# Kernel optimization log

Measured on AMD Instinct MI355X. Metric: run time of the kernel, lower is better.

The kernel has to match this reference:

```python
import jax, jax.numpy as jnp
import numpy as np

N_NODES = 100000
N_EDGES = 1600000
NEG_SLOPE = 0.01  # nn.LeakyReLU default


def gcn_conv(x, edge_index, W, b, n_nodes):
    # PyG GCNConv: h = D^-1/2 (A+I) D^-1/2 (x W) + b
    h = x @ W  # [N, out]
    loops = jnp.arange(n_nodes, dtype=edge_index.dtype)
    src = jnp.concatenate([edge_index[0], loops])
    dst = jnp.concatenate([edge_index[1], loops])
    ones = jnp.ones(src.shape[0], dtype=h.dtype)
    deg = jax.ops.segment_sum(ones, dst, num_segments=n_nodes)  # in-degree incl. self-loop
    dinv = jnp.where(deg > 0, jax.lax.rsqrt(deg), 0.0)
    norm = dinv[src] * dinv[dst]  # [E+N]
    msg = h[src] * norm[:, None]  # gather + scale
    out = jax.ops.segment_sum(msg, dst, num_segments=n_nodes)  # scatter-add
    return out + b


def setup_inputs() -> dict:
    key = jax.random.key(0)
    ks = jax.random.split(key, 8)
    x = jax.random.normal(ks[0], (N_NODES, 128), dtype=jnp.float32)
    edge_index = jax.random.randint(ks[1], (2, N_EDGES), 0, N_NODES, dtype=jnp.int64)
    # Glorot-ish init for params
    W1 = jax.random.normal(ks[2], (128, 64), dtype=jnp.float32) / np.sqrt(128)
    b1 = jnp.zeros((64,), dtype=jnp.float32)
    W2 = jax.random.normal(ks[3], (64, 64), dtype=jnp.float32) / np.sqrt(64)
    b2 = jnp.zeros((64,), dtype=jnp.float32)
    Wfc = jax.random.normal(ks[4], (64, 4), dtype=jnp.float32) / np.sqrt(64)
    bfc = jnp.zeros((4,), dtype=jnp.float32)
    return {"x": x, "edge_index": edge_index, "W1": W1, "b1": b1,
            "W2": W2, "b2": b2, "Wfc": Wfc, "bfc": bfc}


def reference(x, edge_index, W1, b1, W2, b2, Wfc, bfc):
    h = gcn_conv(x, edge_index, W1, b1, N_NODES)
    h = jnp.where(h >= 0, h, NEG_SLOPE * h)  # LeakyReLU
    # F.dropout in eval mode -> identity
    h = gcn_conv(h, edge_index, W2, b2, N_NODES)
    out = h @ Wfc + bfc  # [N, 4]
    return out
```

## Files before the change

### kernel.cpp

```cpp
#include <hip/hip_runtime.h>

#define N_NODES 100000
#define N_EDGES 1600000
#define NEG_SLOPE 0.01f
#define NPAD 102400
#define NBLK_SCAN 391
#define NPART 16
#define PART_SZ 6250
#define CAPP 110000
#define BATCH1 1024
#define NBLK1 1563
#define DCHUNK 8
#define WIN_N 256
#define NWIN 25
#define CAP_B 4608
#define NBKT2 (NPART * NWIN)
#define BATCH1B 1024
#define CHUNK1B 108
#define NBLK1B (NPART * CHUNK1B)
#define CAP_WIN 4608
#define RCAP 768

__device__ inline unsigned pk_bf2(float lo, float hi) {
    unsigned a = __builtin_bit_cast(unsigned, lo);
    unsigned b = __builtin_bit_cast(unsigned, hi);
    a = (a + 0x7fffu + ((a >> 16) & 1u)) >> 16;
    b = (b + 0x7fffu + ((b >> 16) & 1u)) >> 16;
    return a | (b << 16);
}
__device__ inline float ub_lo(unsigned u) { return __builtin_bit_cast(float, u << 16); }
__device__ inline float ub_hi(unsigned u) { return __builtin_bit_cast(float, u & 0xffff0000u); }

__global__ void k_init(int* __restrict__ deg, int* __restrict__ gcur,
                       int* __restrict__ gcur2) {
    int i = blockIdx.x * 256 + threadIdx.x;
    if (i < NPAD) deg[i] = 0;
    if (i < NPART) gcur[i] = i * CAPP;
    if (i < NBKT2) gcur2[i] = i * CAP_B;
}

__global__ __launch_bounds__(256) void k_pass1(const int* __restrict__ src,
                                               const int* __restrict__ dst,
                                               int* __restrict__ gcur,
                                               unsigned* __restrict__ part) {
    __shared__ int hist[NPART];
    __shared__ int scanb[NPART];
    __shared__ int gbase[NPART];
    __shared__ int run[NPART];
    __shared__ unsigned stage[BATCH1];
    const int tid = threadIdx.x;
    const int lane = tid & 63;
    const int e0 = blockIdx.x * BATCH1;
    if (tid < NPART) hist[tid] = 0;
    __syncthreads();
    unsigned rec[4]; int bk[4], rk[4];
    unsigned long long mm[4];
#pragma unroll
    for (int i = 0; i < 4; ++i) {
        int e = e0 + i * 256 + tid;
        if (e < N_EDGES) {
            int d = dst[e];
            int s = src[e];
            int b = d / PART_SZ;
            bk[i] = b;
            rec[i] = ((unsigned)(d - b * PART_SZ) << 17) | (unsigned)s;
        } else bk[i] = -1;
        unsigned long long m = ~0ULL;
#pragma unroll
        for (int bit = 0; bit < 4; ++bit) {
            unsigned long long vote = __ballot((bk[i] >> bit) & 1);
            m &= ((bk[i] >> bit) & 1) ? vote : ~vote;
        }
        m &= __ballot(bk[i] >= 0);
        mm[i] = m;
        rk[i] = __popcll(m & ((1ULL << lane) - 1ULL));
        if (bk[i] >= 0 && rk[i] == 0)
            atomicAdd(&hist[bk[i]], __popcll(m));
    }
    __syncthreads();
    if (tid == 0) {
        int acc = 0;
        for (int b = 0; b < NPART; ++b) { scanb[b] = acc; acc += hist[b]; }
    }
    __syncthreads();
    if (tid < NPART) {
        gbase[tid] = atomicAdd(&gcur[tid], hist[tid]);
        run[tid] = 0;
    }
    __syncthreads();
#pragma unroll
    for (int i = 0; i < 4; ++i) {
        int base_ = 0;
        if (bk[i] >= 0 && rk[i] == 0)
            base_ = atomicAdd(&run[bk[i]], __popcll(mm[i]));
        int leader = mm[i] ? (__ffsll((unsigned long long)mm[i]) - 1) : 0;
        base_ = __shfl(base_, leader);
        if (bk[i] >= 0)
            stage[scanb[bk[i]] + base_ + rk[i]] = rec[i];
    }
    __syncthreads();
    for (int b = 0; b < NPART; ++b) {
        int len = hist[b], sb = scanb[b], gb = gbase[b];
        int lim = (b + 1) * CAPP - gb;
        if (len > lim) len = lim;
        for (int i = tid; i < len; i += 256)
            part[gb + i] = stage[sb + i];
    }
}

__global__ __launch_bounds__(256) void k_pass1b(const unsigned* __restrict__ part,
                                                const int* __restrict__ gcur,
                                                int* __restrict__ gcur2,
                                                unsigned* __restrict__ part2) {
    __shared__ int hist[NWIN];
    __shared__ int scanb[NWIN];
    __shared__ int gbase[NWIN];
    __shared__ int run[NWIN];
    __shared__ unsigned stage[BATCH1B];
    const int p = blockIdx.x & (NPART - 1);
    const int c = blockIdx.x >> 4;
    const int tid = threadIdx.x;
    const int base = p * CAPP;
    int pend = gcur[p]; if (pend > base + CAPP) pend = base + CAPP;
    const int rs = base + c * BATCH1B;
    int re = rs + BATCH1B; if (re > pend) re = pend;
    if (tid < NWIN) { hist[tid] = 0; run[tid] = 0; }
    __syncthreads();
    unsigned rec[4]; int wv[4];
#pragma unroll
    for (int i = 0; i < 4; ++i) {
        int idx = rs + i * 256 + tid;
        if (idx < re) {
            rec[i] = part[idx];
            wv[i] = (int)(rec[i] >> 17) >> 8;
            atomicAdd(&hist[wv[i]], 1);
        } else wv[i] = -1;
    }
    __syncthreads();
    if (tid == 0) {
        int acc = 0;
        for (int w = 0; w < NWIN; ++w) { scanb[w] = acc; acc += hist[w]; }
    }
    __syncthreads();
    if (tid < NWIN) gbase[tid] = atomicAdd(&gcur2[p * NWIN + tid], hist[tid]);
    __syncthreads();
#pragma unroll
    for (int i = 0; i < 4; ++i) {
        if (wv[i] >= 0) {
            int r = atomicAdd(&run[wv[i]], 1);
            stage[scanb[wv[i]] + r] = rec[i];
        }
    }
    __syncthreads();
    for (int w = 0; w < NWIN; ++w) {
        int len = hist[w], sb = scanb[w], gb = gbase[w];
        int lim = (p * NWIN + w + 1) * CAP_B - gb;
        if (len > lim) len = lim;
        for (int i = tid; i < len; i += 256)
            part2[gb + i] = stage[sb + i];
    }
}

__global__ __launch_bounds__(256) void k_degh(const unsigned* __restrict__ part,
                                              const int* __restrict__ gcur,
                                              int* __restrict__ deg) {
    __shared__ int hist[PART_SZ];
    const int p = blockIdx.x & (NPART - 1);
    const int q = blockIdx.x >> 4;
    const int base = p * CAPP;
    int end = gcur[p]; if (end > base + CAPP) end = base + CAPP;
    const int cnt = end - base;
    const int chunksz = (cnt + DCHUNK - 1) / DCHUNK;
    int rs = base + q * chunksz;
    int re = rs + chunksz; if (re > end) re = end;
    for (int i = threadIdx.x; i < PART_SZ; i += 256) hist[i] = 0;
    __syncthreads();
    for (int i = rs + threadIdx.x; i < re; i += 256)
        atomicAdd(&hist[part[i] >> 17], 1);
    __syncthreads();
    const int pbase = p * PART_SZ;
    for (int i = threadIdx.x; i < PART_SZ; i += 256) {
        int v = hist[i];
        if (v) atomicAdd(&deg[pbase + i], v);
    }
}

__global__ __launch_bounds__(256) void k_scan1(const int* __restrict__ deg,
                                               int* __restrict__ cur,
                                               int* __restrict__ bsum,
                                               float* __restrict__ dinv) {
    __shared__ int sd[256];
    int t = threadIdx.x;
    int gid = blockIdx.x * 256 + t;
    int v = (gid < N_NODES) ? deg[gid] : 0;
    dinv[gid] = rsqrtf((float)(v + 1));
    sd[t] = v;
    __syncthreads();
    for (int off = 1; off < 256; off <<= 1) {
        int add = (t >= off) ? sd[t - off] : 0;
        __syncthreads();
        sd[t] += add;
        __syncthreads();
    }
    cur[gid] = sd[t] - v;
    if (t == 255) bsum[blockIdx.x] = sd[255];
}
// ... 42 lines not shown
    if (tid == 0) {
        int acc = 0;
        for (int i = 0; i < nwin; ++i) { lofs[i] = acc; acc += lcnt[i]; }
        lofs[nwin] = acc;
    }
    __syncthreads();
    const int pbase = p * PART_SZ;
    const int wbase = cur[pbase + dlo];
    for (int i = bs + tid; i < be; i += 256) {
        unsigned rc = part2[i];
        int dl = (int)(rc >> 17);
        int s = rc & 0x1FFFF;
        int n = pbase + dl;
        float wgt = dinv[s] * dinv[n];
        int pos = lofs[dl - dlo] + atomicAdd(&lrun[dl - dlo], 1);
        uint2 r = make_uint2((unsigned)s, __builtin_bit_cast(unsigned, wgt));
        if (pos < CAP_WIN) stage[pos] = r;
        else csr8[wbase + pos] = r;
    }
    __syncthreads();
    int total = lofs[nwin]; if (total > CAP_WIN) total = CAP_WIN;
    for (int i = tid; i < total; i += 256)
        csr8[wbase + i] = stage[i];
}

__global__ __launch_bounds__(256) void k_gemm_bf(const float* __restrict__ X,
                                                 const float* __restrict__ W,
                                                 unsigned* __restrict__ Y) {
    __shared__ float ws[128 * 64];
    const int tid = threadIdx.x;
    const int row0 = blockIdx.x * 64;
    for (int i = tid; i < 2048; i += 256)
        ((float4*)ws)[i] = ((const float4*)W)[i];
    __syncthreads();
    const int cg = tid & 15, rg = tid >> 4;
    const int c0 = cg * 4;
    const float4* Xv = (const float4*)X;
    size_t rb0, rb1, rb2, rb3;
    {
        int row = row0 + rg * 4;
        rb0 = (size_t)((row     < N_NODES) ? row     : (N_NODES - 1)) * 32;
        rb1 = (size_t)((row + 1 < N_NODES) ? row + 1 : (N_NODES - 1)) * 32;
        rb2 = (size_t)((row + 2 < N_NODES) ? row + 2 : (N_NODES - 1)) * 32;
        rb3 = (size_t)((row + 3 < N_NODES) ? row + 3 : (N_NODES - 1)) * 32;
    }
    float acc[4][4] = {};
    float4 xa0 = Xv[rb0], xa1 = Xv[rb1], xa2 = Xv[rb2], xa3 = Xv[rb3];
#pragma unroll 1
    for (int kq = 0; kq < 32; kq += 2) {
        float4 xb0 = Xv[rb0 + kq + 1], xb1 = Xv[rb1 + kq + 1];
        float4 xb2 = Xv[rb2 + kq + 1], xb3 = Xv[rb3 + kq + 1];
        {
            const int k = kq * 4;
            float4 w0 = *(const float4*)&ws[(k + 0) * 64 + c0];
            float4 w1 = *(const float4*)&ws[(k + 1) * 64 + c0];
            float4 w2 = *(const float4*)&ws[(k + 2) * 64 + c0];
            float4 w3 = *(const float4*)&ws[(k + 3) * 64 + c0];
            float4 xv;
            xv = xa0;
            acc[0][0] = fmaf(xv.x, w0.x, acc[0][0]); acc[0][1] = fmaf(xv.x, w0.y, acc[0][1]);
            acc[0][2] = fmaf(xv.x, w0.z, acc[0][2]); acc[0][3] = fmaf(xv.x, w0.w, acc[0][3]);
            acc[0][0] = fmaf(xv.y, w1.x, acc[0][0]); acc[0][1] = fmaf(xv.y, w1.y, acc[0][1]);
            acc[0][2] = fmaf(xv.y, w1.z, acc[0][2]); acc[0][3] = fmaf(xv.y, w1.w, acc[0][3]);
            acc[0][0] = fmaf(xv.z, w2.x, acc[0][0]); acc[0][1] = fmaf(xv.z, w2.y, acc[0][1]);
            acc[0][2] = fmaf(xv.z, w2.z, acc[0][2]); acc[0][3] = fmaf(xv.z, w2.w, acc[0][3]);
            acc[0][0] = fmaf(xv.w, w3.x, acc[0][0]); acc[0][1] = fmaf(xv.w, w3.y, acc[0][1]);
            acc[0][2] = fmaf(xv.w, w3.z, acc[0][2]); acc[0][3] = fmaf(xv.w, w3.w, acc[0][3]);
            xv = xa1;
            acc[1][0] = fmaf(xv.x, w0.x, acc[1][0]); acc[1][1] = fmaf(xv.x, w0.y, acc[1][1]);
            acc[1][2] = fmaf(xv.x, w0.z, acc[1][2]); acc[1][3] = fmaf(xv.x, w0.w, acc[1][3]);
            acc[1][0] = fmaf(xv.y, w1.x, acc[1][0]); acc[1][1] = fmaf(xv.y, w1.y, acc[1][1]);
            acc[1][2] = fmaf(xv.y, w1.z, acc[1][2]); acc[1][3] = fmaf(xv.y, w1.w, acc[1][3]);
            acc[1][0] = fmaf(xv.z, w2.x, acc[1][0]); acc[1][1] = fmaf(xv.z, w2.y, acc[1][1]);
            acc[1][2] = fmaf(xv.z, w2.z, acc[1][2]); acc[1][3] = fmaf(xv.z, w2.w, acc[1][3]);
            acc[1][0] = fmaf(xv.w, w3.x, acc[1][0]); acc[1][1] = fmaf(xv.w, w3.y, acc[1][1]);
            acc[1][2] = fmaf(xv.w, w3.z, acc[1][2]); acc[1][3] = fmaf(xv.w, w3.w, acc[1][3]);
            xv = xa2;
            acc[2][0] = fmaf(xv.x, w0.x, acc[2][0]); acc[2][1] = fmaf(xv.x, w0.y, acc[2][1]);
            acc[2][2] = fmaf(xv.x, w0.z, acc[2][2]); acc[2][3] = fmaf(xv.x, w0.w, acc[2][3]);
            acc[2][0] = fmaf(xv.y, w1.x, acc[2][0]); acc[2][1] = fmaf(xv.y, w1.y, acc[2][1]);
            acc[2][2] = fmaf(xv.y, w1.z, acc[2][2]); acc[2][3] = fmaf(xv.y, w1.w, acc[2][3]);
            acc[2][0] = fmaf(xv.z, w2.x, acc[2][0]); acc[2][1] = fmaf(xv.z, w2.y, acc[2][1]);
            acc[2][2] = fmaf(xv.z, w2.z, acc[2][2]); acc[2][3] = fmaf(xv.z, w2.w, acc[2][3]);
            acc[2][0] = fmaf(xv.w, w3.x, acc[2][0]); acc[2][1] = fmaf(xv.w, w3.y, acc[2][1]);
            acc[2][2] = fmaf(xv.w, w3.z, acc[2][2]); acc[2][3] = fmaf(xv.w, w3.w, acc[2][3]);
            xv = xa3;
            acc[3][0] = fmaf(xv.x, w0.x, acc[3][0]); acc[3][1] = fmaf(xv.x, w0.y, acc[3][1]);
            acc[3][2] = fmaf(xv.x, w0.z, acc[3][2]); acc[3][3] = fmaf(xv.x, w0.w, acc[3][3]);
            acc[3][0] = fmaf(xv.y, w1.x, acc[3][0]); acc[3][1] = fmaf(xv.y, w1.y, acc[3][1]);
            acc[3][2] = fmaf(xv.y, w1.z, acc[3][2]); acc[3][3] = fmaf(xv.y, w1.w, acc[3][3]);
            acc[3][0] = fmaf(xv.z, w2.x, acc[3][0]); acc[3][1] = fmaf(xv.z, w2.y, acc[3][1]);
            acc[3][2] = fmaf(xv.z, w2.z, acc[3][2]); acc[3][3] = fmaf(xv.z, w2.w, acc[3][3]);
            acc[3][0] = fmaf(xv.w, w3.x, acc[3][0]); acc[3][1] = fmaf(xv.w, w3.y, acc[3][1]);
            acc[3][2] = fmaf(xv.w, w3.z, acc[3][2]); acc[3][3] = fmaf(xv.w, w3.w, acc[3][3]);
        }
        if (kq + 2 < 32) {
            xa0 = Xv[rb0 + kq + 2]; xa1 = Xv[rb1 + kq + 2];
            xa2 = Xv[rb2 + kq + 2]; xa3 = Xv[rb3 + kq + 2];
        }
        {
            const int k = (kq + 1) * 4;
            float4 w0 = *(const float4*)&ws[(k + 0) * 64 + c0];
            float4 w1 = *(const float4*)&ws[(k + 1) * 64 + c0];
            float4 w2 = *(const float4*)&ws[(k + 2) * 64 + c0];
            float4 w3 = *(const float4*)&ws[(k + 3) * 64 + c0];
            float4 xv;
            xv = xb0;
            acc[0][0] = fmaf(xv.x, w0.x, acc[0][0]); acc[0][1] = fmaf(xv.x, w0.y, acc[0][1]);
            acc[0][2] = fmaf(xv.x, w0.z, acc[0][2]); acc[0][3] = fmaf(xv.x, w0.w, acc[0][3]);
            acc[0][0] = fmaf(xv.y, w1.x, acc[0][0]); acc[0][1] = fmaf(xv.y, w1.y, acc[0][1]);
            acc[0][2] = fmaf(xv.y, w1.z, acc[0][2]); acc[0][3] = fmaf(xv.y, w1.w, acc[0][3]);
            acc[0][0] = fmaf(xv.z, w2.x, acc[0][0]); acc[0][1] = fmaf(xv.z, w2.y, acc[0][1]);
            acc[0][2] = fmaf(xv.z, w2.z, acc[0][2]); acc[0][3] = fmaf(xv.z, w2.w, acc[0][3]);
            acc[0][0] = fmaf(xv.w, w3.x, acc[0][0]); acc[0][1] = fmaf(xv.w, w3.y, acc[0][1]);
            acc[0][2] = fmaf(xv.w, w3.z, acc[0][2]); acc[0][3] = fmaf(xv.w, w3.w, acc[0][3]);
            xv = xb1;
            acc[1][0] = fmaf(xv.x, w0.x, acc[1][0]); acc[1][1] = fmaf(xv.x, w0.y, acc[1][1]);
            acc[1][2] = fmaf(xv.x, w0.z, acc[1][2]); acc[1][3] = fmaf(xv.x, w0.w, acc[1][3]);
            acc[1][0] = fmaf(xv.y, w1.x, acc[1][0]); acc[1][1] = fmaf(xv.y, w1.y, acc[1][1]);
            acc[1][2] = fmaf(xv.y, w1.z, acc[1][2]); acc[1][3] = fmaf(xv.y, w1.w, acc[1][3]);
            acc[1][0] = fmaf(xv.z, w2.x, acc[1][0]); acc[1][1] = fmaf(xv.z, w2.y, acc[1][1]);
            acc[1][2] = fmaf(xv.z, w2.z, acc[1][2]); acc[1][3] = fmaf(xv.z, w2.w, acc[1][3]);
            acc[1][0] = fmaf(xv.w, w3.x, acc[1][0]); acc[1][1] = fmaf(xv.w, w3.y, acc[1][1]);
            acc[1][2] = fmaf(xv.w, w3.z, acc[1][2]); acc[1][3] = fmaf(xv.w, w3.w, acc[1][3]);
            xv = xb2;
            acc[2][0] = fmaf(xv.x, w0.x, acc[2][0]); acc[2][1] = fmaf(xv.x, w0.y, acc[2][1]);
            acc[2][2] = fmaf(xv.x, w0.z, acc[2][2]); acc[2][3] = fmaf(xv.x, w0.w, acc[2][3]);
            acc[2][0] = fmaf(xv.y, w1.x, acc[2][0]); acc[2][1] = fmaf(xv.y, w1.y, acc[2][1]);
            acc[2][2] = fmaf(xv.y, w1.z, acc[2][2]); acc[2][3] = fmaf(xv.y, w1.w, acc[2][3]);
            acc[2][0] = fmaf(xv.z, w2.x, acc[2][0]); acc[2][1] = fmaf(xv.z, w2.y, acc[2][1]);
            acc[2][2] = fmaf(xv.z, w2.z, acc[2][2]); acc[2][3] = fmaf(xv.z, w2.w, acc[2][3]);
            acc[2][0] = fmaf(xv.w, w3.x, acc[2][0]); acc[2][1] = fmaf(xv.w, w3.y, acc[2][1]);
            acc[2][2] = fmaf(xv.w, w3.z, acc[2][2]); acc[2][3] = fmaf(xv.w, w3.w, acc[2][3]);
            xv = xb3;
            acc[3][0] = fmaf(xv.x, w0.x, acc[3][0]); acc[3][1] = fmaf(xv.x, w0.y, acc[3][1]);
            acc[3][2] = fmaf(xv.x, w0.z, acc[3][2]); acc[3][3] = fmaf(xv.x, w0.w, acc[3][3]);
            acc[3][0] = fmaf(xv.y, w1.x, acc[3][0]); acc[3][1] = fmaf(xv.y, w1.y, acc[3][1]);
            acc[3][2] = fmaf(xv.y, w1.z, acc[3][2]); acc[3][3] = fmaf(xv.y, w1.w, acc[3][3]);
            acc[3][0] = fmaf(xv.z, w2.x, acc[3][0]); acc[3][1] = fmaf(xv.z, w2.y, acc[3][1]);
            acc[3][2] = fmaf(xv.z, w2.z, acc[3][2]); acc[3][3] = fmaf(xv.z, w2.w, acc[3][3]);
            acc[3][0] = fmaf(xv.w, w3.x, acc[3][0]); acc[3][1] = fmaf(xv.w, w3.y, acc[3][1]);
            acc[3][2] = fmaf(xv.w, w3.z, acc[3][2]); acc[3][3] = fmaf(xv.w, w3.w, acc[3][3]);
        }
    }
#pragma unroll
    for (int j = 0; j < 4; ++j) {
        int row = row0 + rg * 4 + j;
        if (row < N_NODES) {
            uint2 v;
            v.x = pk_bf2(acc[j][0], acc[j][1]);
            v.y = pk_bf2(acc[j][2], acc[j][3]);
            *(uint2*)&Y[(size_t)row * 32 + cg * 2] = v;
        }
    }
}

__global__ __launch_bounds__(256) void k_foldw(const float* __restrict__ W2,
                                               const float* __restrict__ b2,
                                               const float* __restrict__ Wfc,
                                               const float* __restrict__ bfc,
                                               float* __restrict__ Wc,
                                               float* __restrict__ cfold) {
    __shared__ float wf[64 * 4];
    int tid = threadIdx.x;
    wf[tid] = Wfc[tid];
    __syncthreads();
    int k = tid >> 2, c = tid & 3;
    float acc = 0.f;
#pragma unroll
    for (int j = 0; j < 64; ++j) acc = fmaf(W2[k * 64 + j], wf[j * 4 + c], acc);
    Wc[k * 4 + c] = acc;
    if (tid < 4) {
        float s = bfc[tid];
        for (int j = 0; j < 64; ++j) s = fmaf(b2[j], wf[j * 4 + tid], s);
        cfold[tid] = s;
    }
}

__global__ __launch_bounds__(256) void k_agg_bf2(const int* __restrict__ cur,
                                                 const uint2* __restrict__ csr8,
                                                 const float* __restrict__ dinv,
                                                 const unsigned* __restrict__ hb,
                                                 const float* __restrict__ b,
                                                 const float* __restrict__ Wc,
                                                 float* __restrict__ G) {
    __shared__ uint2 rec[RCAP];
    __shared__ int scur[17];
    const int tid = threadIdx.x;
    const int base = blockIdx.x * 16;
    if (tid < 17) scur[tid] = cur[base + tid];
    __syncthreads();
    const int bstart = scur[0];
    const int total = scur[16] - bstart;
    const int staged = (total < RCAP) ? total : RCAP;
    for (int i = tid; i < staged; i += 256) rec[i] = csr8[bstart + i];
    __syncthreads();
    const int lane = tid & 63, wv = tid >> 6;
    const int sub = lane & 31, half = lane >> 5;
    for (int nn = wv; nn < 16; nn += 4) {
// ... 190 lines not shown
    const float* W2  = (const float*)d_in[4];
    const float* b2  = (const float*)d_in[5];
    const float* Wfc = (const float*)d_in[6];
    const float* bfc = (const float*)d_in[7];
    float* out = (float*)d_out;

    int*      deg   = (int*)d_ws;
    int*      cur   = deg + NPAD;
    float*    dinv  = (float*)(cur + NPAD);
    int*      bsum  = (int*)(dinv + NPAD);
    float*    Wc    = (float*)(bsum + 1024);
    float*    cfold = Wc + 256;
    int*      gcur  = (int*)(cfold + 256);
    int*      gcur2 = gcur + 256;
    unsigned* part  = (unsigned*)(gcur2 + 512);
    unsigned* part2 = part + (size_t)NPART * CAPP;
    uint2*    csr8  = (uint2*)(part2 + (size_t)NBKT2 * CAP_B);
    unsigned* hb    = (unsigned*)(csr8 + N_EDGES);
    float*    G     = (float*)(hb + (size_t)N_NODES * 32);

    const int* src = ei;
    const int* dst = ei + N_EDGES;

    k_init<<<(NPAD + 255) / 256, 256, 0, stream>>>(deg, gcur, gcur2);

    k_pass1<<<NBLK1, 256, 0, stream>>>(src, dst, gcur, part);

    k_pass1b<<<NBLK1B, 256, 0, stream>>>(part, gcur, gcur2, part2);

    k_degh<<<NPART * DCHUNK, 256, 0, stream>>>(part, gcur, deg);

    k_scan1<<<NBLK_SCAN, 256, 0, stream>>>(deg, cur, bsum, dinv);
    k_scan2<<<1, 512, 0, stream>>>(bsum);
    k_scan3<<<NBLK_SCAN, 256, 0, stream>>>(cur, bsum);

    k_pass2c<<<NBKT2, 256, 0, stream>>>(part2, gcur2, dinv, cur, csr8);

    k_foldw<<<1, 256, 0, stream>>>(W2, b2, Wfc, bfc, Wc, cfold);

    k_gemm_bf<<<(N_NODES + 63) / 64, 256, 0, stream>>>(x, W1, hb);
    k_agg_bf2<<<N_NODES / 16, 256, 0, stream>>>(cur, csr8, dinv, hb, b1, Wc, G);

    k_agg4<<<(N_NODES + 255) / 256, 256, 0, stream>>>(cur, csr8, dinv,
                                                      (const float4*)G, cfold,
                                                      (float4*)out);
}
```

Baseline: 175.7 us.

## Merge independent kernels into shared launches via block-index dispatch

Independent stages are combined into single launches whose blocks branch on blockIdx. The weight-folding kernel joins the init kernel, the GEMM on x joins the first partition pass, and the second partition pass joins the degree histogram. This cuts the number of launches and lets unrelated work overlap on the device. The cost is higher shared-memory and register demand in the combined kernels, since each block must reserve the larger footprint, which may lower occupancy for the lighter branch.

```diff
diff --git a/kernel.cpp b/kernel.cpp
--- a/kernel.cpp
+++ b/kernel.cpp
@@ -10,14 +10,14 @@
 #define CAPP 110000
 #define BATCH1 1024
 #define NBLK1 1563
+#define NBLKG 1563
 #define DCHUNK 8
 #define WIN_N 256
 #define NWIN 25
 #define CAP_B 4608
 #define NBKT2 (NPART * NWIN)
 #define BATCH1B 1024
-#define CHUNK1B 108
-#define NBLK1B (NPART * CHUNK1B)
+#define NBLK1B 1728
 #define CAP_WIN 4608
 #define RCAP 768
 
@@ -31,157 +31,314 @@
 __device__ inline float ub_lo(unsigned u) { return __builtin_bit_cast(float, u << 16); }
 __device__ inline float ub_hi(unsigned u) { return __builtin_bit_cast(float, u & 0xffff0000u); }
 
-__global__ void k_init(int* __restrict__ deg, int* __restrict__ gcur,
-                       int* __restrict__ gcur2) {
-    int i = blockIdx.x * 256 + threadIdx.x;
-    if (i < NPAD) deg[i] = 0;
-    if (i < NPART) gcur[i] = i * CAPP;
-    if (i < NBKT2) gcur2[i] = i * CAP_B;
-}
-
-__global__ __launch_bounds__(256) void k_pass1(const int* __restrict__ src,
-                                               const int* __restrict__ dst,
-                                               int* __restrict__ gcur,
-                                               unsigned* __restrict__ part) {
-    __shared__ int hist[NPART];
-    __shared__ int scanb[NPART];
-    __shared__ int gbase[NPART];
-    __shared__ int run[NPART];
-    __shared__ unsigned stage[BATCH1];
+__global__ __launch_bounds__(256) void k_init(int* __restrict__ deg,
+                                              int* __restrict__ gcur,
+                                              int* __restrict__ gcur2,
+                                              const float* __restrict__ W2,
+                                              const float* __restrict__ b2,
+                                              const float* __restrict__ Wfc,
+                                              const float* __restrict__ bfc,
+                                              float* __restrict__ Wc,
+                                              float* __restrict__ cfold) {
+    __shared__ float wf[64 * 4];
     const int tid = threadIdx.x;
-    const int lane = tid & 63;
-    const int e0 = blockIdx.x * BATCH1;
-    if (tid < NPART) hist[tid] = 0;
-    __syncthreads();
-    unsigned rec[4]; int bk[4], rk[4];
-    unsigned long long mm[4];
-#pragma unroll
-    for (int i = 0; i < 4; ++i) {
-        int e = e0 + i * 256 + tid;
-        if (e < N_EDGES) {
-            int d = dst[e];
-            int s = src[e];
-            int b = d / PART_SZ;
-            bk[i] = b;
-            rec[i] = ((unsigned)(d - b * PART_SZ) << 17) | (unsigned)s;
-        } else bk[i] = -1;
-        unsigned long long m = ~0ULL;
-#pragma unroll
-        for (int bit = 0; bit < 4; ++bit) {
-            unsigned long long vote = __ballot((bk[i] >> bit) & 1);
-            m &= ((bk[i] >> bit) & 1) ? vote : ~vote;
-        }
-        m &= __ballot(bk[i] >= 0);
-        mm[i] = m;
-        rk[i] = __popcll(m & ((1ULL << lane) - 1ULL));
-        if (bk[i] >= 0 && rk[i] == 0)
-            atomicAdd(&hist[bk[i]], __popcll(m));
-    }
-    __syncthreads();
-    if (tid == 0) {
-        int acc = 0;
-        for (int b = 0; b < NPART; ++b) { scanb[b] = acc; acc += hist[b]; }
-    }
-    __syncthreads();
-    if (tid < NPART) {
-        gbase[tid] = atomicAdd(&gcur[tid], hist[tid]);
-        run[tid] = 0;
-    }
-    __syncthreads();
-#pragma unroll
-    for (int i = 0; i < 4; ++i) {
-        int base_ = 0;
-        if (bk[i] >= 0 && rk[i] == 0)
-            base_ = atomicAdd(&run[bk[i]], __popcll(mm[i]));
-        int leader = mm[i] ? (__ffsll((unsigned long long)mm[i]) - 1) : 0;
-        base_ = __shfl(base_, leader);
-        if (bk[i] >= 0)
-            stage[scanb[bk[i]] + base_ + rk[i]] = rec[i];
-    }
-    __syncthreads();
-    for (int b = 0; b < NPART; ++b) {
-        int len = hist[b], sb = scanb[b], gb = gbase[b];
-        int lim = (b + 1) * CAPP - gb;
-        if (len > lim) len = lim;
-        for (int i = tid; i < len; i += 256)
-            part[gb + i] = stage[sb + i];
-    }
-}
-
-__global__ __launch_bounds__(256) void k_pass1b(const unsigned* __restrict__ part,
-                                                const int* __restrict__ gcur,
-                                                int* __restrict__ gcur2,
-                                                unsigned* __restrict__ part2) {
-    __shared__ int hist[NWIN];
-    __shared__ int scanb[NWIN];
-    __shared__ int gbase[NWIN];
-    __shared__ int run[NWIN];
-    __shared__ unsigned stage[BATCH1B];
-    const int p = blockIdx.x & (NPART - 1);
-    const int c = blockIdx.x >> 4;
+    if (blockIdx.x < 400) {
+        int i = blockIdx.x * 256 + tid;
+        if (i < NPAD) deg[i] = 0;
+        if (i < NPART) gcur[i] = i * CAPP;
+        if (i < NBKT2) gcur2[i] = i * CAP_B;
+    } else {
+        wf[tid] = Wfc[tid];
+        __syncthreads();
+        int k = tid >> 2, c = tid & 3;
+        float acc = 0.f;
+#pragma unroll
+        for (int j = 0; j < 64; ++j) acc = fmaf(W2[k * 64 + j], wf[j * 4 + c], acc);
+        Wc[k * 4 + c] = acc;
+        if (tid < 4) {
+            float s = bfc[tid];
+            for (int j = 0; j < 64; ++j) s = fmaf(b2[j], wf[j * 4 + tid], s);
+            cfold[tid] = s;
+        }
+    }
+}
+
+__global__ __launch_bounds__(256) void k_p1gemm(const int* __restrict__ src,
+                                                const int* __restrict__ dst,
+                                                int* __restrict__ gcur,
+                                                unsigned* __restrict__ part,
+                                                const float* __restrict__ X,
+                                                const float* __restrict__ W,
+                                                unsigned* __restrict__ Y) {
+    __shared__ __align__(16) unsigned smem[8192];
     const int tid = threadIdx.x;
-    const int base = p * CAPP;
-    int pend = gcur[p]; if (pend > base + CAPP) pend = base + CAPP;
-    const int rs = base + c * BATCH1B;
-    int re = rs + BATCH1B; if (re > pend) re = pend;
-    if (tid < NWIN) { hist[tid] = 0; run[tid] = 0; }
-    __syncthreads();
-    unsigned rec[4]; int wv[4];
-#pragma unroll
-    for (int i = 0; i < 4; ++i) {
-        int idx = rs + i * 256 + tid;
-        if (idx < re) {
-            rec[i] = part[idx];
-            wv[i] = (int)(rec[i] >> 17) >> 8;
-            atomicAdd(&hist[wv[i]], 1);
-        } else wv[i] = -1;
-    }
-    __syncthreads();
-    if (tid == 0) {
-        int acc = 0;
-        for (int w = 0; w < NWIN; ++w) { scanb[w] = acc; acc += hist[w]; }
-    }
-    __syncthreads();
-    if (tid < NWIN) gbase[tid] = atomicAdd(&gcur2[p * NWIN + tid], hist[tid]);
-    __syncthreads();
-#pragma unroll
-    for (int i = 0; i < 4; ++i) {
-        if (wv[i] >= 0) {
-            int r = atomicAdd(&run[wv[i]], 1);
-            stage[scanb[wv[i]] + r] = rec[i];
-        }
-    }
-    __syncthreads();
-    for (int w = 0; w < NWIN; ++w) {
-        int len = hist[w], sb = scanb[w], gb = gbase[w];
-        int lim = (p * NWIN + w + 1) * CAP_B - gb;
-        if (len > lim) len = lim;
-        for (int i = tid; i < len; i += 256)
-            part2[gb + i] = stage[sb + i];
-    }
-}
-
-__global__ __launch_bounds__(256) void k_degh(const unsigned* __restrict__ part,
-                                              const int* __restrict__ gcur,
-                                              int* __restrict__ deg) {
-    __shared__ int hist[PART_SZ];
-    const int p = blockIdx.x & (NPART - 1);
-    const int q = blockIdx.x >> 4;
-    const int base = p * CAPP;
-    int end = gcur[p]; if (end > base + CAPP) end = base + CAPP;
-    const int cnt = end - base;
-    const int chunksz = (cnt + DCHUNK - 1) / DCHUNK;
-    int rs = base + q * chunksz;
-    int re = rs + chunksz; if (re > end) re = end;
-    for (int i = threadIdx.x; i < PART_SZ; i += 256) hist[i] = 0;
-    __syncthreads();
-    for (int i = rs + threadIdx.x; i < re; i += 256)
-        atomicAdd(&hist[part[i] >> 17], 1);
-    __syncthreads();
-    const int pbase = p * PART_SZ;
-    for (int i = threadIdx.x; i < PART_SZ; i += 256) {
-        int v = hist[i];
-        if (v) atomicAdd(&deg[pbase + i], v);
+    if (blockIdx.x < NBLK1) {
+        int* hist  = (int*)smem;
+        int* scanb = hist + 16;
+        int* gbase = hist + 32;
+        int* run   = hist + 48;
+        unsigned* stage = smem + 64;
+        const int lane = tid & 63;
+        const int e0 = blockIdx.x * BATCH1;
+        if (tid < NPART) hist[tid] = 0;
+        __syncthreads();
+        unsigned rec[4]; int bk[4], rk[4];
+        unsigned long long mm[4];
+#pragma unroll
+        for (int i = 0; i < 4; ++i) {
+            int e = e0 + i * 256 + tid;
+            if (e < N_EDGES) {
+                int d = dst[e];
+                int s = src[e];
+                int b = d / PART_SZ;
+                bk[i] = b;
+                rec[i] = ((unsigned)(d - b * PART_SZ) << 17) | (unsigned)s;
+            } else bk[i] = -1;
+            unsigned long long m = ~0ULL;
+#pragma unroll
+            for (int bit = 0; bit < 4; ++bit) {
+                unsigned long long vote = __ballot((bk[i] >> bit) & 1);
+                m &= ((bk[i] >> bit) & 1) ? vote : ~vote;
+            }
+            m &= __ballot(bk[i] >= 0);
+            mm[i] = m;
+            rk[i] = __popcll(m & ((1ULL << lane) - 1ULL));
+            if (bk[i] >= 0 && rk[i] == 0)
+                atomicAdd(&hist[bk[i]], __popcll(m));
+        }
+        __syncthreads();
+        if (tid == 0) {
+            int acc = 0;
+            for (int b = 0; b < NPART; ++b) { scanb[b] = acc; acc += hist[b]; }
+        }
+        __syncthreads();
+        if (tid < NPART) {
+            gbase[tid] = atomicAdd(&gcur[tid], hist[tid]);
+            run[tid] = 0;
+        }
+        __syncthreads();
+#pragma unroll
+        for (int i = 0; i < 4; ++i) {
+            int base_ = 0;
+            if (bk[i] >= 0 && rk[i] == 0)
+                base_ = atomicAdd(&run[bk[i]], __popcll(mm[i]));
+            int leader = mm[i] ? (__ffsll((unsigned long long)mm[i]) - 1) : 0;
+            base_ = __shfl(base_, leader);
+            if (bk[i] >= 0)
+                stage[scanb[bk[i]] + base_ + rk[i]] = rec[i];
+        }
+        __syncthreads();
+        for (int b = 0; b < NPART; ++b) {
+            int len = hist[b], sb = scanb[b], gb = gbase[b];
+            int lim = (b + 1) * CAPP - gb;
+            if (len > lim) len = lim;
+            for (int i = tid; i < len; i += 256)
+                part[gb + i] = stage[sb + i];
+        }
+    } else {
+        float* ws = (float*)smem;
+        const int row0 = (blockIdx.x - NBLK1) * 64;
+        for (int i = tid; i < 2048; i += 256)
+            ((float4*)ws)[i] = ((const float4*)W)[i];
+        __syncthreads();
+        const int cg = tid & 15, rg = tid >> 4;
+        const int c0 = cg * 4;
+        const float4* Xv = (const float4*)X;
+        size_t rb0, rb1, rb2, rb3;
+        {
+            int row = row0 + rg * 4;
+            rb0 = (size_t)((row     < N_NODES) ? row     : (N_NODES - 1)) * 32;
+            rb1 = (size_t)((row + 1 < N_NODES) ? row + 1 : (N_NODES - 1)) * 32;
+            rb2 = (size_t)((row + 2 < N_NODES) ? row + 2 : (N_NODES - 1)) * 32;
+            rb3 = (size_t)((row + 3 < N_NODES) ? row + 3 : (N_NODES - 1)) * 32;
+        }
+        float acc[4][4] = {};
+        float4 xa0 = Xv[rb0], xa1 = Xv[rb1], xa2 = Xv[rb2], xa3 = Xv[rb3];
+#pragma unroll 1
+        for (int kq = 0; kq < 32; kq += 2) {
+            float4 xb0 = Xv[rb0 + kq + 1], xb1 = Xv[rb1 + kq + 1];
+            float4 xb2 = Xv[rb2 + kq + 1], xb3 = Xv[rb3 + kq + 1];
+            {
+                const int k = kq * 4;
+                float4 w0 = *(const float4*)&ws[(k + 0) * 64 + c0];
+                float4 w1 = *(const float4*)&ws[(k + 1) * 64 + c0];
+                float4 w2 = *(const float4*)&ws[(k + 2) * 64 + c0];
+                float4 w3 = *(const float4*)&ws[(k + 3) * 64 + c0];
+                float4 xv;
+                xv = xa0;
+                acc[0][0] = fmaf(xv.x, w0.x, acc[0][0]); acc[0][1] = fmaf(xv.x, w0.y, acc[0][1]);
+                acc[0][2] = fmaf(xv.x, w0.z, acc[0][2]); acc[0][3] = fmaf(xv.x, w0.w, acc[0][3]);
+                acc[0][0] = fmaf(xv.y, w1.x, acc[0][0]); acc[0][1] = fmaf(xv.y, w1.y, acc[0][1]);
+                acc[0][2] = fmaf(xv.y, w1.z, acc[0][2]); acc[0][3] = fmaf(xv.y, w1.w, acc[0][3]);
+                acc[0][0] = fmaf(xv.z, w2.x, acc[0][0]); acc[0][1] = fmaf(xv.z, w2.y, acc[0][1]);
+                acc[0][2] = fmaf(xv.z, w2.z, acc[0][2]); acc[0][3] = fmaf(xv.z, w2.w, acc[0][3]);
+                acc[0][0] = fmaf(xv.w, w3.x, acc[0][0]); acc[0][1] = fmaf(xv.w, w3.y, acc[0][1]);
+                acc[0][2] = fmaf(xv.w, w3.z, acc[0][2]); acc[0][3] = fmaf(xv.w, w3.w, acc[0][3]);
+                xv = xa1;
+                acc[1][0] = fmaf(xv.x, w0.x, acc[1][0]); acc[1][1] = fmaf(xv.x, w0.y, acc[1][1]);
+                acc[1][2] = fmaf(xv.x, w0.z, acc[1][2]); acc[1][3] = fmaf(xv.x, w0.w, acc[1][3]);
+                acc[1][0] = fmaf(xv.y, w1.x, acc[1][0]); acc[1][1] = fmaf(xv.y, w1.y, acc[1][1]);
+                acc[1][2] = fmaf(xv.y, w1.z, acc[1][2]); acc[1][3] = fmaf(xv.y, w1.w, acc[1][3]);
+                acc[1][0] = fmaf(xv.z, w2.x, acc[1][0]); acc[1][1] = fmaf(xv.z, w2.y, acc[1][1]);
+                acc[1][2] = fmaf(xv.z, w2.z, acc[1][2]); acc[1][3] = fmaf(xv.z, w2.w, acc[1][3]);
+                acc[1][0] = fmaf(xv.w, w3.x, acc[1][0]); acc[1][1] = fmaf(xv.w, w3.y, acc[1][1]);
+                acc[1][2] = fmaf(xv.w, w3.z, acc[1][2]); acc[1][3] = fmaf(xv.w, w3.w, acc[1][3]);
+                xv = xa2;
+                acc[2][0] = fmaf(xv.x, w0.x, acc[2][0]); acc[2][1] = fmaf(xv.x, w0.y, acc[2][1]);
+                acc[2][2] = fmaf(xv.x, w0.z, acc[2][2]); acc[2][3] = fmaf(xv.x, w0.w, acc[2][3]);
+                acc[2][0] = fmaf(xv.y, w1.x, acc[2][0]); acc[2][1] = fmaf(xv.y, w1.y, acc[2][1]);
+                acc[2][2] = fmaf(xv.y, w1.z, acc[2][2]); acc[2][3] = fmaf(xv.y, w1.w, acc[2][3]);
+                acc[2][0] = fmaf(xv.z, w2.x, acc[2][0]); acc[2][1] = fmaf(xv.z, w2.y, acc[2][1]);
+                acc[2][2] = fmaf(xv.z, w2.z, acc[2][2]); acc[2][3] = fmaf(xv.z, w2.w, acc[2][3]);
+                acc[2][0] = fmaf(xv.w, w3.x, acc[2][0]); acc[2][1] = fmaf(xv.w, w3.y, acc[2][1]);
+                acc[2][2] = fmaf(xv.w, w3.z, acc[2][2]); acc[2][3] = fmaf(xv.w, w3.w, acc[2][3]);
+                xv = xa3;
+                acc[3][0] = fmaf(xv.x, w0.x, acc[3][0]); acc[3][1] = fmaf(xv.x, w0.y, acc[3][1]);
+                acc[3][2] = fmaf(xv.x, w0.z, acc[3][2]); acc[3][3] = fmaf(xv.x, w0.w, acc[3][3]);
+                acc[3][0] = fmaf(xv.y, w1.x, acc[3][0]); acc[3][1] = fmaf(xv.y, w1.y, acc[3][1]);
+                acc[3][2] = fmaf(xv.y, w1.z, acc[3][2]); acc[3][3] = fmaf(xv.y, w1.w, acc[3][3]);
+                acc[3][0] = fmaf(xv.z, w2.x, acc[3][0]); acc[3][1] = fmaf(xv.z, w2.y, acc[3][1]);
+                acc[3][2] = fmaf(xv.z, w2.z, acc[3][2]); acc[3][3] = fmaf(xv.z, w2.w, acc[3][3]);
+                acc[3][0] = fmaf(xv.w, w3.x, acc[3][0]); acc[3][1] = fmaf(xv.w, w3.y, acc[3][1]);
+                acc[3][2] = fmaf(xv.w, w3.z, acc[3][2]); acc[3][3] = fmaf(xv.w, w3.w, acc[3][3]);
+            }
+            if (kq + 2 < 32) {
+                xa0 = Xv[rb0 + kq + 2]; xa1 = Xv[rb1 + kq + 2];
+                xa2 = Xv[rb2 + kq + 2]; xa3 = Xv[rb3 + kq + 2];
+            }
+            {
+                const int k = (kq + 1) * 4;
+                float4 w0 = *(const float4*)&ws[(k + 0) * 64 + c0];
+                float4 w1 = *(const float4*)&ws[(k + 1) * 64 + c0];
+                float4 w2 = *(const float4*)&ws[(k + 2) * 64 + c0];
+                float4 w3 = *(const float4*)&ws[(k + 3) * 64 + c0];
+                float4 xv;
+                xv = xb0;
+                acc[0][0] = fmaf(xv.x, w0.x, acc[0][0]); acc[0][1] = fmaf(xv.x, w0.y, acc[0][1]);
+                acc[0][2] = fmaf(xv.x, w0.z, acc[0][2]); acc[0][3] = fmaf(xv.x, w0.w, acc[0][3]);
+                acc[0][0] = fmaf(xv.y, w1.x, acc[0][0]); acc[0][1] = fmaf(xv.y, w1.y, acc[0][1]);
+                acc[0][2] = fmaf(xv.y, w1.z, acc[0][2]); acc[0][3] = fmaf(xv.y, w1.w, acc[0][3]);
+                acc[0][0] = fmaf(xv.z, w2.x, acc[0][0]); acc[0][1] = fmaf(xv.z, w2.y, acc[0][1]);
+                acc[0][2] = fmaf(xv.z, w2.z, acc[0][2]); acc[0][3] = fmaf(xv.z, w2.w, acc[0][3]);
+                acc[0][0] = fmaf(xv.w, w3.x, acc[0][0]); acc[0][1] = fmaf(xv.w, w3.y, acc[0][1]);
+                acc[0][2] = fmaf(xv.w, w3.z, acc[0][2]); acc[0][3] = fmaf(xv.w, w3.w, acc[0][3]);
+                xv = xb1;
+                acc[1][0] = fmaf(xv.x, w0.x, acc[1][0]); acc[1][1] = fmaf(xv.x, w0.y, acc[1][1]);
+                acc[1][2] = fmaf(xv.x, w0.z, acc[1][2]); acc[1][3] = fmaf(xv.x, w0.w, acc[1][3]);
+                acc[1][0] = fmaf(xv.y, w1.x, acc[1][0]); acc[1][1] = fmaf(xv.y, w1.y, acc[1][1]);
+                acc[1][2] = fmaf(xv.y, w1.z, acc[1][2]); acc[1][3] = fmaf(xv.y, w1.w, acc[1][3]);
+                acc[1][0] = fmaf(xv.z, w2.x, acc[1][0]); acc[1][1] = fmaf(xv.z, w2.y, acc[1][1]);
+                acc[1][2] = fmaf(xv.z, w2.z, acc[1][2]); acc[1][3] = fmaf(xv.z, w2.w, acc[1][3]);
+                acc[1][0] = fmaf(xv.w, w3.x, acc[1][0]); acc[1][1] = fmaf(xv.w, w3.y, acc[1][1]);
+                acc[1][2] = fmaf(xv.w, w3.z, acc[1][2]); acc[1][3] = fmaf(xv.w, w3.w, acc[1][3]);
+                xv = xb2;
+                acc[2][0] = fmaf(xv.x, w0.x, acc[2][0]); acc[2][1] = fmaf(xv.x, w0.y, acc[2][1]);
+                acc[2][2] = fmaf(xv.x, w0.z, acc[2][2]); acc[2][3] = fmaf(xv.x, w0.w, acc[2][3]);
+                acc[2][0] = fmaf(xv.y, w1.x, acc[2][0]); acc[2][1] = fmaf(xv.y, w1.y, acc[2][1]);
+                acc[2][2] = fmaf(xv.y, w1.z, acc[2][2]); acc[2][3] = fmaf(xv.y, w1.w, acc[2][3]);
+                acc[2][0] = fmaf(xv.z, w2.x, acc[2][0]); acc[2][1] = fmaf(xv.z, w2.y, acc[2][1]);
+                acc[2][2] = fmaf(xv.z, w2.z, acc[2][2]); acc[2][3] = fmaf(xv.z, w2.w, acc[2][3]);
+                acc[2][0] = fmaf(xv.w, w3.x, acc[2][0]); acc[2][1] = fmaf(xv.w, w3.y, acc[2][1]);
+                acc[2][2] = fmaf(xv.w, w3.z, acc[2][2]); acc[2][3] = fmaf(xv.w, w3.w, acc[2][3]);
+                xv = xb3;
+                acc[3][0] = fmaf(xv.x, w0.x, acc[3][0]); acc[3][1] = fmaf(xv.x, w0.y, acc[3][1]);
+                acc[3][2] = fmaf(xv.x, w0.z, acc[3][2]); acc[3][3] = fmaf(xv.x, w0.w, acc[3][3]);
+                acc[3][0] = fmaf(xv.y, w1.x, acc[3][0]); acc[3][1] = fmaf(xv.y, w1.y, acc[3][1]);
+                acc[3][2] = fmaf(xv.y, w1.z, acc[3][2]); acc[3][3] = fmaf(xv.y, w1.w, acc[3][3]);
+                acc[3][0] = fmaf(xv.z, w2.x, acc[3][0]); acc[3][1] = fmaf(xv.z, w2.y, acc[3][1]);
+                acc[3][2] = fmaf(xv.z, w2.z, acc[3][2]); acc[3][3] = fmaf(xv.z, w2.w, acc[3][3]);
+                acc[3][0] = fmaf(xv.w, w3.x, acc[3][0]); acc[3][1] = fmaf(xv.w, w3.y, acc[3][1]);
+                acc[3][2] = fmaf(xv.w, w3.z, acc[3][2]); acc[3][3] = fmaf(xv.w, w3.w, acc[3][3]);
+            }
+        }
+#pragma unroll
+        for (int j = 0; j < 4; ++j) {
+            int row = row0 + rg * 4 + j;
+            if (row < N_NODES) {
+                uint2 v;
+                v.x = pk_bf2(acc[j][0], acc[j][1]);
+                v.y = pk_bf2(acc[j][2], acc[j][3]);
+                *(uint2*)&Y[(size_t)row * 32 + cg * 2] = v;
+            }
+        }
+    }
+}
+
+__global__ __launch_bounds__(256) void k_p1bdegh(const unsigned* __restrict__ part,
+                                                 const int* __restrict__ gcur,
+                                                 int* __restrict__ gcur2,
+                                                 unsigned* __restrict__ part2,
+                                                 int* __restrict__ deg) {
+    __shared__ __align__(16) int smem[PART_SZ];
+    const int tid = threadIdx.x;
+    if (blockIdx.x < NBLK1B) {
+        int* hist  = smem;
+        int* scanb = smem + 32;
+        int* gbase = smem + 64;
+        int* run   = smem + 96;
+        unsigned* stage = (unsigned*)(smem + 128);
+        const int p = blockIdx.x & (NPART - 1);
+        const int c = blockIdx.x >> 4;
+        const int base = p * CAPP;
+        int pend = gcur[p]; if (pend > base + CAPP) pend = base + CAPP;
+        const int rs = base + c * BATCH1B;
+        int re = rs + BATCH1B; if (re > pend) re = pend;
+        if (tid < NWIN) { hist[tid] = 0; run[tid] = 0; }
+        __syncthreads();
+        unsigned rec[4]; int wv[4];
+#pragma unroll
+        for (int i = 0; i < 4; ++i) {
+            int idx = rs + i * 256 + tid;
+            if (idx < re) {
+                rec[i] = part[idx];
+                wv[i] = (int)(rec[i] >> 17) >> 8;
+                atomicAdd(&hist[wv[i]], 1);
+            } else wv[i] = -1;
+        }
+        __syncthreads();
+        if (tid == 0) {
+            int acc = 0;
+            for (int w = 0; w < NWIN; ++w) { scanb[w] = acc; acc += hist[w]; }
+        }
+        __syncthreads();
+        if (tid < NWIN) gbase[tid] = atomicAdd(&gcur2[p * NWIN + tid], hist[tid]);
+        __syncthreads();
+#pragma unroll
+        for (int i = 0; i < 4; ++i) {
+            if (wv[i] >= 0) {
+                int r = atomicAdd(&run[wv[i]], 1);
+                stage[scanb[wv[i]] + r] = rec[i];
+            }
+        }
+        __syncthreads();
+        for (int w = 0; w < NWIN; ++w) {
+            int len = hist[w], sb = scanb[w], gb = gbase[w];
+            int lim = (p * NWIN + w + 1) * CAP_B - gb;
+            if (len > lim) len = lim;
+            for (int i = tid; i < len; i += 256)
+                part2[gb + i] = stage[sb + i];
+        }
+    } else {
+        int* hist = smem;
+        const int b2 = blockIdx.x - NBLK1B;
+        const int p = b2 & (NPART - 1);
+        const int q = b2 >> 4;
+        const int base = p * CAPP;
+        int end = gcur[p]; if (end > base + CAPP) end = base + CAPP;
+        const int cnt = end - base;
+        const int chunksz = (cnt + DCHUNK - 1) / DCHUNK;
+        int rs = base + q * chunksz;
+        int re = rs + chunksz; if (re > end) re = end;
+        for (int i = tid; i < PART_SZ; i += 256) hist[i] = 0;
+        __syncthreads();
+        for (int i = rs + tid; i < re; i += 256)
+            atomicAdd(&hist[part[i] >> 17], 1);
+        __syncthreads();
+        const int pbase = p * PART_SZ;
+        for (int i = tid; i < PART_SZ; i += 256) {
+            int v = hist[i];
+            if (v) atomicAdd(&deg[pbase + i], v);
+        }
     }
 }
 
@@ -270,159 +427,6 @@
     int total = lofs[nwin]; if (total > CAP_WIN) total = CAP_WIN;
     for (int i = tid; i < total; i += 256)
         csr8[wbase + i] = stage[i];
-}
-
-__global__ __launch_bounds__(256) void k_gemm_bf(const float* __restrict__ X,
-                                                 const float* __restrict__ W,
-                                                 unsigned* __restrict__ Y) {
-    __shared__ float ws[128 * 64];
-    const int tid = threadIdx.x;
-    const int row0 = blockIdx.x * 64;
-    for (int i = tid; i < 2048; i += 256)
-        ((float4*)ws)[i] = ((const float4*)W)[i];
-    __syncthreads();
-    const int cg = tid & 15, rg = tid >> 4;
-    const int c0 = cg * 4;
-    const float4* Xv = (const float4*)X;
-    size_t rb0, rb1, rb2, rb3;
-    {
-        int row = row0 + rg * 4;
-        rb0 = (size_t)((row     < N_NODES) ? row     : (N_NODES - 1)) * 32;
-        rb1 = (size_t)((row + 1 < N_NODES) ? row + 1 : (N_NODES - 1)) * 32;
-        rb2 = (size_t)((row + 2 < N_NODES) ? row + 2 : (N_NODES - 1)) * 32;
-        rb3 = (size_t)((row + 3 < N_NODES) ? row + 3 : (N_NODES - 1)) * 32;
-    }
-    float acc[4][4] = {};
-    float4 xa0 = Xv[rb0], xa1 = Xv[rb1], xa2 = Xv[rb2], xa3 = Xv[rb3];
-#pragma unroll 1
-    for (int kq = 0; kq < 32; kq += 2) {
-        float4 xb0 = Xv[rb0 + kq + 1], xb1 = Xv[rb1 + kq + 1];
-        float4 xb2 = Xv[rb2 + kq + 1], xb3 = Xv[rb3 + kq + 1];
-        {
-            const int k = kq * 4;
-            float4 w0 = *(const float4*)&ws[(k + 0) * 64 + c0];
-            float4 w1 = *(const float4*)&ws[(k + 1) * 64 + c0];
-            float4 w2 = *(const float4*)&ws[(k + 2) * 64 + c0];
-            float4 w3 = *(const float4*)&ws[(k + 3) * 64 + c0];
-            float4 xv;
-            xv = xa0;
-            acc[0][0] = fmaf(xv.x, w0.x, acc[0][0]); acc[0][1] = fmaf(xv.x, w0.y, acc[0][1]);
-            acc[0][2] = fmaf(xv.x, w0.z, acc[0][2]); acc[0][3] = fmaf(xv.x, w0.w, acc[0][3]);
-            acc[0][0] = fmaf(xv.y, w1.x, acc[0][0]); acc[0][1] = fmaf(xv.y, w1.y, acc[0][1]);
-            acc[0][2] = fmaf(xv.y, w1.z, acc[0][2]); acc[0][3] = fmaf(xv.y, w1.w, acc[0][3]);
-            acc[0][0] = fmaf(xv.z, w2.x, acc[0][0]); acc[0][1] = fmaf(xv.z, w2.y, acc[0][1]);
-            acc[0][2] = fmaf(xv.z, w2.z, acc[0][2]); acc[0][3] = fmaf(xv.z, w2.w, acc[0][3]);
-            acc[0][0] = fmaf(xv.w, w3.x, acc[0][0]); acc[0][1] = fmaf(xv.w, w3.y, acc[0][1]);
-            acc[0][2] = fmaf(xv.w, w3.z, acc[0][2]); acc[0][3] = fmaf(xv.w, w3.w, acc[0][3]);
-            xv = xa1;
-            acc[1][0] = fmaf(xv.x, w0.x, acc[1][0]); acc[1][1] = fmaf(xv.x, w0.y, acc[1][1]);
-            acc[1][2] = fmaf(xv.x, w0.z, acc[1][2]); acc[1][3] = fmaf(xv.x, w0.w, acc[1][3]);
-            acc[1][0] = fmaf(xv.y, w1.x, acc[1][0]); acc[1][1] = fmaf(xv.y, w1.y, acc[1][1]);
-            acc[1][2] = fmaf(xv.y, w1.z, acc[1][2]); acc[1][3] = fmaf(xv.y, w1.w, acc[1][3]);
-            acc[1][0] = fmaf(xv.z, w2.x, acc[1][0]); acc[1][1] = fmaf(xv.z, w2.y, acc[1][1]);
-            acc[1][2] = fmaf(xv.z, w2.z, acc[1][2]); acc[1][3] = fmaf(xv.z, w2.w, acc[1][3]);
-            acc[1][0] = fmaf(xv.w, w3.x, acc[1][0]); acc[1][1] = fmaf(xv.w, w3.y, acc[1][1]);
-            acc[1][2] = fmaf(xv.w, w3.z, acc[1][2]); acc[1][3] = fmaf(xv.w, w3.w, acc[1][3]);
-            xv = xa2;
-            acc[2][0] = fmaf(xv.x, w0.x, acc[2][0]); acc[2][1] = fmaf(xv.x, w0.y, acc[2][1]);
-            acc[2][2] = fmaf(xv.x, w0.z, acc[2][2]); acc[2][3] = fmaf(xv.x, w0.w, acc[2][3]);
-            acc[2][0] = fmaf(xv.y, w1.x, acc[2][0]); acc[2][1] = fmaf(xv.y, w1.y, acc[2][1]);
-            acc[2][2] = fmaf(xv.y, w1.z, acc[2][2]); acc[2][3] = fmaf(xv.y, w1.w, acc[2][3]);
-            acc[2][0] = fmaf(xv.z, w2.x, acc[2][0]); acc[2][1] = fmaf(xv.z, w2.y, acc[2][1]);
-            acc[2][2] = fmaf(xv.z, w2.z, acc[2][2]); acc[2][3] = fmaf(xv.z, w2.w, acc[2][3]);
-            acc[2][0] = fmaf(xv.w, w3.x, acc[2][0]); acc[2][1] = fmaf(xv.w, w3.y, acc[2][1]);
-            acc[2][2] = fmaf(xv.w, w3.z, acc[2][2]); acc[2][3] = fmaf(xv.w, w3.w, acc[2][3]);
-            xv = xa3;
-            acc[3][0] = fmaf(xv.x, w0.x, acc[3][0]); acc[3][1] = fmaf(xv.x, w0.y, acc[3][1]);
-            acc[3][2] = fmaf(xv.x, w0.z, acc[3][2]); acc[3][3] = fmaf(xv.x, w0.w, acc[3][3]);
-            acc[3][0] = fmaf(xv.y, w1.x, acc[3][0]); acc[3][1] = fmaf(xv.y, w1.y, acc[3][1]);
-            acc[3][2] = fmaf(xv.y, w1.z, acc[3][2]); acc[3][3] = fmaf(xv.y, w1.w, acc[3][3]);
-            acc[3][0] = fmaf(xv.z, w2.x, acc[3][0]); acc[3][1] = fmaf(xv.z, w2.y, acc[3][1]);
-            acc[3][2] = fmaf(xv.z, w2.z, acc[3][2]); acc[3][3] = fmaf(xv.z, w2.w, acc[3][3]);
-            acc[3][0] = fmaf(xv.w, w3.x, acc[3][0]); acc[3][1] = fmaf(xv.w, w3.y, acc[3][1]);
-            acc[3][2] = fmaf(xv.w, w3.z, acc[3][2]); acc[3][3] = fmaf(xv.w, w3.w, acc[3][3]);
-        }
-        if (kq + 2 < 32) {
-            xa0 = Xv[rb0 + kq + 2]; xa1 = Xv[rb1 + kq + 2];
-            xa2 = Xv[rb2 + kq + 2]; xa3 = Xv[rb3 + kq + 2];
-        }
-        {
-            const int k = (kq + 1) * 4;
-            float4 w0 = *(const float4*)&ws[(k + 0) * 64 + c0];
-            float4 w1 = *(const float4*)&ws[(k + 1) * 64 + c0];
-            float4 w2 = *(const float4*)&ws[(k + 2) * 64 + c0];
-            float4 w3 = *(const float4*)&ws[(k + 3) * 64 + c0];
-            float4 xv;
-            xv = xb0;
-            acc[0][0] = fmaf(xv.x, w0.x, acc[0][0]); acc[0][1] = fmaf(xv.x, w0.y, acc[0][1]);
-            acc[0][2] = fmaf(xv.x, w0.z, acc[0][2]); acc[0][3] = fmaf(xv.x, w0.w, acc[0][3]);
-            acc[0][0] = fmaf(xv.y, w1.x, acc[0][0]); acc[0][1] = fmaf(xv.y, w1.y, acc[0][1]);
-            acc[0][2] = fmaf(xv.y, w1.z, acc[0][2]); acc[0][3] = fmaf(xv.y, w1.w, acc[0][3]);
-            acc[0][0] = fmaf(xv.z, w2.x, acc[0][0]); acc[0][1] = fmaf(xv.z, w2.y, acc[0][1]);
-            acc[0][2] = fmaf(xv.z, w2.z, acc[0][2]); acc[0][3] = fmaf(xv.z, w2.w, acc[0][3]);
-            acc[0][0] = fmaf(xv.w, w3.x, acc[0][0]); acc[0][1] = fmaf(xv.w, w3.y, acc[0][1]);
-            acc[0][2] = fmaf(xv.w, w3.z, acc[0][2]); acc[0][3] = fmaf(xv.w, w3.w, acc[0][3]);
-            xv = xb1;
-            acc[1][0] = fmaf(xv.x, w0.x, acc[1][0]); acc[1][1] = fmaf(xv.x, w0.y, acc[1][1]);
-            acc[1][2] = fmaf(xv.x, w0.z, acc[1][2]); acc[1][3] = fmaf(xv.x, w0.w, acc[1][3]);
-            acc[1][0] = fmaf(xv.y, w1.x, acc[1][0]); acc[1][1] = fmaf(xv.y, w1.y, acc[1][1]);
-            acc[1][2] = fmaf(xv.y, w1.z, acc[1][2]); acc[1][3] = fmaf(xv.y, w1.w, acc[1][3]);
-            acc[1][0] = fmaf(xv.z, w2.x, acc[1][0]); acc[1][1] = fmaf(xv.z, w2.y, acc[1][1]);
-            acc[1][2] = fmaf(xv.z, w2.z, acc[1][2]); acc[1][3] = fmaf(xv.z, w2.w, acc[1][3]);
-            acc[1][0] = fmaf(xv.w, w3.x, acc[1][0]); acc[1][1] = fmaf(xv.w, w3.y, acc[1][1]);
-            acc[1][2] = fmaf(xv.w, w3.z, acc[1][2]); acc[1][3] = fmaf(xv.w, w3.w, acc[1][3]);
-            xv = xb2;
-            acc[2][0] = fmaf(xv.x, w0.x, acc[2][0]); acc[2][1] = fmaf(xv.x, w0.y, acc[2][1]);
-            acc[2][2] = fmaf(xv.x, w0.z, acc[2][2]); acc[2][3] = fmaf(xv.x, w0.w, acc[2][3]);
-            acc[2][0] = fmaf(xv.y, w1.x, acc[2][0]); acc[2][1] = fmaf(xv.y, w1.y, acc[2][1]);
-            acc[2][2] = fmaf(xv.y, w1.z, acc[2][2]); acc[2][3] = fmaf(xv.y, w1.w, acc[2][3]);
-            acc[2][0] = fmaf(xv.z, w2.x, acc[2][0]); acc[2][1] = fmaf(xv.z, w2.y, acc[2][1]);
-            acc[2][2] = fmaf(xv.z, w2.z, acc[2][2]); acc[2][3] = fmaf(xv.z, w2.w, acc[2][3]);
-            acc[2][0] = fmaf(xv.w, w3.x, acc[2][0]); acc[2][1] = fmaf(xv.w, w3.y, acc[2][1]);
-            acc[2][2] = fmaf(xv.w, w3.z, acc[2][2]); acc[2][3] = fmaf(xv.w, w3.w, acc[2][3]);
-            xv = xb3;
-            acc[3][0] = fmaf(xv.x, w0.x, acc[3][0]); acc[3][1] = fmaf(xv.x, w0.y, acc[3][1]);
-            acc[3][2] = fmaf(xv.x, w0.z, acc[3][2]); acc[3][3] = fmaf(xv.x, w0.w, acc[3][3]);
-            acc[3][0] = fmaf(xv.y, w1.x, acc[3][0]); acc[3][1] = fmaf(xv.y, w1.y, acc[3][1]);
-            acc[3][2] = fmaf(xv.y, w1.z, acc[3][2]); acc[3][3] = fmaf(xv.y, w1.w, acc[3][3]);
-            acc[3][0] = fmaf(xv.z, w2.x, acc[3][0]); acc[3][1] = fmaf(xv.z, w2.y, acc[3][1]);
-            acc[3][2] = fmaf(xv.z, w2.z, acc[3][2]); acc[3][3] = fmaf(xv.z, w2.w, acc[3][3]);
-            acc[3][0] = fmaf(xv.w, w3.x, acc[3][0]); acc[3][1] = fmaf(xv.w, w3.y, acc[3][1]);
-            acc[3][2] = fmaf(xv.w, w3.z, acc[3][2]); acc[3][3] = fmaf(xv.w, w3.w, acc[3][3]);
-        }
-    }
-#pragma unroll
-    for (int j = 0; j < 4; ++j) {
-        int row = row0 + rg * 4 + j;
-        if (row < N_NODES) {
-            uint2 v;
-            v.x = pk_bf2(acc[j][0], acc[j][1]);
-            v.y = pk_bf2(acc[j][2], acc[j][3]);
-            *(uint2*)&Y[(size_t)row * 32 + cg * 2] = v;
-        }
-    }
-}
-
-__global__ __launch_bounds__(256) void k_foldw(const float* __restrict__ W2,
-                                               const float* __restrict__ b2,
-                                               const float* __restrict__ Wfc,
-                                               const float* __restrict__ bfc,
-                                               float* __restrict__ Wc,
-                                               float* __restrict__ cfold) {
-    __shared__ float wf[64 * 4];
-    int tid = threadIdx.x;
-    wf[tid] = Wfc[tid];
-    __syncthreads();
-    int k = tid >> 2, c = tid & 3;
-    float acc = 0.f;
-#pragma unroll
-    for (int j = 0; j < 64; ++j) acc = fmaf(W2[k * 64 + j], wf[j * 4 + c], acc);
-    Wc[k * 4 + c] = acc;
-    if (tid < 4) {
-        float s = bfc[tid];
-        for (int j = 0; j < 64; ++j) s = fmaf(b2[j], wf[j * 4 + tid], s);
-        cfold[tid] = s;
-    }
 }
 
 __global__ __launch_bounds__(256) void k_agg_bf2(const int* __restrict__ cur,
@@ -659,13 +663,12 @@
     const int* src = ei;
     const int* dst = ei + N_EDGES;
 
-    k_init<<<(NPAD + 255) / 256, 256, 0, stream>>>(deg, gcur, gcur2);
-
-    k_pass1<<<NBLK1, 256, 0, stream>>>(src, dst, gcur, part);
-
-    k_pass1b<<<NBLK1B, 256, 0, stream>>>(part, gcur, gcur2, part2);
-
-    k_degh<<<NPART * DCHUNK, 256, 0, stream>>>(part, gcur, deg);
+    k_init<<<401, 256, 0, stream>>>(deg, gcur, gcur2, W2, b2, Wfc, bfc, Wc, cfold);
+
+    k_p1gemm<<<NBLK1 + NBLKG, 256, 0, stream>>>(src, dst, gcur, part, x, W1, hb);
+
+    k_p1bdegh<<<NBLK1B + NPART * DCHUNK, 256, 0, stream>>>(part, gcur, gcur2,
+                                                           part2, deg);
 
     k_scan1<<<NBLK_SCAN, 256, 0, stream>>>(deg, cur, bsum, dinv);
     k_scan2<<<1, 512, 0, stream>>>(bsum);
@@ -673,9 +676,6 @@
 
     k_pass2c<<<NBKT2, 256, 0, stream>>>(part2, gcur2, dinv, cur, csr8);
 
-    k_foldw<<<1, 256, 0, stream>>>(W2, b2, Wfc, bfc, Wc, cfold);
-
-    k_gemm_bf<<<(N_NODES + 63) / 64, 256, 0, stream>>>(x, W1, hb);
     k_agg_bf2<<<N_NODES / 16, 256, 0, stream>>>(cur, csr8, dinv, hb, b1, Wc, G);
 
     k_agg4<<<(N_NODES + 255) / 256, 256, 0, stream>>>(cur, csr8, dinv,
```

Result: faster. 161.5 us (-8.1%).
